# Optimization experiments

Hardware: AMD Instinct MI355X
Metric: run time of the kernel (lower is better)

Reference implementation:

```python
import jax, jax.numpy as jnp
import numpy as np

WINDOW = 7
SHIFT = 3
HEADS = 4


def _rel_pos_index(w):
    # same construction as ShiftedWindowAttention.__init__ (numpy, static)
    coords = np.stack(np.meshgrid(np.arange(w), np.arange(w), indexing='ij'))  # [2,w,w]
    cf = coords.reshape(2, -1)                       # [2, w*w]
    rc = (cf[:, :, None] - cf[:, None, :]).transpose(1, 2, 0)  # [L,L,2]
    rc[:, :, 0] += w - 1
    rc[:, :, 1] += w - 1
    rc[:, :, 0] *= 2 * w - 1
    return rc.sum(-1).reshape(-1)                    # [L*L]


def _attn_mask(H, W, w, s):
    # cyclic-shift attention mask, static numpy constant
    m = np.zeros((H, W))
    slices = ((0, -w), (-w, -s), (-s, None))
    cnt = 0
    for hs in slices:
        for ws in slices:
            m[hs[0]:hs[1], ws[0]:ws[1]] = cnt
            cnt += 1
    m = m.reshape(H // w, w, W // w, w).transpose(0, 2, 1, 3).reshape(-1, w * w)  # [nwin, L]
    d = m[:, None, :] - m[:, :, None]                # [nwin, L, L]
    return np.where(d != 0, -100.0, 0.0).astype(np.float32)


def setup_inputs() -> dict:
    key = jax.random.key(0)
    ks = jax.random.split(key, 6)
    B, H, W, C = 64, 56, 56, 128
    return {
        'x': jax.random.normal(ks[0], (B, H, W, C), dtype=jnp.float32),
        'qkv_weight': jax.random.normal(ks[1], (3 * C, C), dtype=jnp.float32) * 0.02,
        'qkv_bias': jax.random.normal(ks[2], (3 * C,), dtype=jnp.float32) * 0.02,
        'proj_weight': jax.random.normal(ks[3], (C, C), dtype=jnp.float32) * 0.02,
        'proj_bias': jax.random.normal(ks[4], (C,), dtype=jnp.float32) * 0.02,
        'rel_bias_table': jax.random.normal(ks[5], ((2 * WINDOW - 1) ** 2, HEADS), dtype=jnp.float32) * 0.02,
    }


def reference(x, qkv_weight, qkv_bias, proj_weight, proj_bias, rel_bias_table):
    B, H, W, C = x.shape
    w, s, h = WINDOW, SHIFT, HEADS
    d = C // h
    nH, nW = H // w, W // w
    nwin = nH * nW
    L = w * w

    # relative position bias: [h, L, L]
    bias = rel_bias_table[jnp.asarray(_rel_pos_index(w))].reshape(L, L, h).transpose(2, 0, 1)

    # cyclic shift + window partition -> [B*nwin, L, C]
    xs = jnp.roll(x, (-s, -s), axis=(1, 2))
    xw = xs.reshape(B, nH, w, nW, w, C).transpose(0, 1, 3, 2, 4, 5).reshape(B * nwin, L, C)

    # fused qkv projection (F.linear: x @ W.T + b)
    qkv = (xw @ qkv_weight.T + qkv_bias).reshape(B * nwin, L, 3, h, d).transpose(2, 0, 3, 1, 4)
    q, k, v = qkv[0] * (d ** -0.5), qkv[1], qkv[2]   # each [B*nwin, h, L, d]

    attn = jnp.einsum('nhqd,nhkd->nhqk', q, k) + bias[None]
    mask = jnp.asarray(_attn_mask(H, W, w, s))       # [nwin, L, L]
    attn = attn.reshape(B, nwin, h, L, L) + mask[None, :, None]
    attn = jax.nn.softmax(attn.reshape(B * nwin, h, L, L), axis=-1)

    out = jnp.einsum('nhqk,nhkd->nhqd', attn, v).transpose(0, 2, 1, 3).reshape(B * nwin, L, C)
    out = out @ proj_weight.T + proj_bias

    # window merge + reverse shift -> [B, H, W, C]
    out = out.reshape(B, nH, nW, w, w, C).transpose(0, 1, 3, 2, 4, 5).reshape(B, H, W, C)
    return jnp.roll(out, (s, s), axis=(1, 2))
```

## Files before the change

### kernel.cpp

```cpp
#include <hip/hip_runtime.h>

typedef __attribute__((ext_vector_type(8))) short short8;
typedef __attribute__((ext_vector_type(4))) float f32x4;

static __device__ __forceinline__ unsigned short f2bf(float f) {
  union { float f; unsigned int u; } v; v.f = f;
  unsigned int r = v.u + 0x7FFFu + ((v.u >> 16) & 1u);
  return (unsigned short)(r >> 16);
}
static __device__ __forceinline__ unsigned int pack2(float a, float b) {
  return (unsigned int)f2bf(a) | ((unsigned int)f2bf(b) << 16);
}

#define B1 0
#define B2 2560
#define WS2 5120

__global__ __launch_bounds__(256) void k_prep(const float* __restrict__ wq,
    const float* __restrict__ wp, const float* __restrict__ tbl,
    unsigned short* __restrict__ dq, unsigned short* __restrict__ dp,
    unsigned short* __restrict__ biasH) {
  const int n = blockIdx.x * 256 + threadIdx.x;
  if (n < 384 * 128) dq[n] = f2bf(wq[n]);
  if (n < 128 * 128) dp[n] = f2bf(wp[n]);
  if (n < 65536) {
    const int j = n & 63, i = (n >> 6) & 63;
    const int h = (n >> 12) & 3, bb = (n >> 14) & 1, aa = (n >> 15) & 1;
    float val;
    if (i >= 49) val = 0.0f;
    else if (j >= 49) val = -1e30f;
    else {
      const int ih = i / 7, iw = i - ih * 7, jh = j / 7, jw = j - jh * 7;
      const int didx = (ih - jh + 6) * 13 + (iw - jw + 6);
      const int irg = (aa ? (ih < 4 ? 3 : 6) : 0) + (bb ? (iw < 4 ? 1 : 2) : 0);
      const int jrg = (aa ? (jh < 4 ? 3 : 6) : 0) + (bb ? (jw < 4 ? 1 : 2) : 0);
      val = tbl[didx * 4 + h] - (irg != jrg ? 100.0f : 0.0f);
    }
    biasH[n] = f2bf(val);
  }
}

__global__ __launch_bounds__(256, 2) void k_fused(const float* __restrict__ x,
    const unsigned short* __restrict__ Wq, const float* __restrict__ qb,
    const unsigned short* __restrict__ Wp, const float* __restrict__ pb,
    const unsigned short* __restrict__ biasH, float* __restrict__ out) {
  __shared__ __align__(16) unsigned short lds[4 * WS2];
  const int tid = threadIdx.x;
  const int win = blockIdx.x;
  const int b = win >> 6, wl = win & 63;
  const int wh = wl >> 3, ww = wl & 7;
  const int wv = tid >> 6, ln = tid & 63;
  const int l15 = ln & 15, l4 = ln >> 4;
  unsigned short* W = lds + wv * WS2;

  const unsigned short* bmB = biasH
      + ((((wh == 7 ? 2 : 0) + (ww == 7 ? 1 : 0)) * 4 + wv) << 12)
      + l15 * 64 + 4 * l4;
  uint2 bm16[4][4];
#pragma unroll
  for (int mt = 0; mt < 4; ++mt)
#pragma unroll
    for (int nt = 0; nt < 4; ++nt)
      bm16[mt][nt] = *(const uint2*)(bmB + mt * 1024 + nt * 16);
  __builtin_amdgcn_sched_barrier(0);

  const float* rp[4];
  bool vld[4];
#pragma unroll
  for (int mt = 0; mt < 4; ++mt) {
    const int t = mt * 16 + l15;
    vld[mt] = (t < 49);
    const int tc = vld[mt] ? t : 0;
    const int th = tc / 7, tw = tc - th * 7;
    int sh = wh * 7 + th + 3; if (sh >= 56) sh -= 56;
    int sw = ww * 7 + tw + 3; if (sw >= 56) sw -= 56;
    rp[mt] = x + (((size_t)(b * 56 + sh)) * 56 + sw) * 128;
  }
  int nrow[6];
#pragma unroll
  for (int j = 0; j < 6; ++j)
    nrow[j] = (j >> 1) * 128 + wv * 32 + (j & 1) * 16 + l15;

  const f32x4 z4 = {0.f, 0.f, 0.f, 0.f};
  f32x4 aS[4][4], aV[4][2];
#pragma unroll
  for (int mt = 0; mt < 4; ++mt) {
#pragma unroll
    for (int j = 0; j < 4; ++j) aS[mt][j] = z4;
#pragma unroll
    for (int j = 0; j < 2; ++j) aV[mt][j] = z4;
  }
#pragma unroll
  for (int ks = 0; ks < 4; ++ks) {
    short8 af[4], bf[6];
#pragma unroll
    for (int mt = 0; mt < 4; ++mt) {
      const float4* p = (const float4*)(rp[mt] + ks * 32 + l4 * 8);
      float4 fa = p[0], fb = p[1];
      uint4 u;
      u.x = pack2(fa.x, fa.y); u.y = pack2(fa.z, fa.w);
      u.z = pack2(fb.x, fb.y); u.w = pack2(fb.z, fb.w);
      u.x = vld[mt] ? u.x : 0u; u.y = vld[mt] ? u.y : 0u;
      u.z = vld[mt] ? u.z : 0u; u.w = vld[mt] ? u.w : 0u;
      af[mt] = *(short8*)&u;
    }
#pragma unroll
    for (int j = 0; j < 6; ++j)
      bf[j] = *(const short8*)&Wq[(size_t)nrow[j] * 128 + ks * 32 + l4 * 8];
#pragma unroll
    for (int mt = 0; mt < 4; ++mt) {
#pragma unroll
      for (int j = 0; j < 4; ++j)
        aS[mt][j] = __builtin_amdgcn_mfma_f32_16x16x32_bf16(bf[j], af[mt], aS[mt][j], 0, 0, 0);
#pragma unroll
      for (int j = 0; j < 2; ++j)
        aV[mt][j] = __builtin_amdgcn_mfma_f32_16x16x32_bf16(af[mt], bf[4 + j], aV[mt][j], 0, 0, 0);
    }
  }
  {
    const float SC = 0.17677669529663687f;
    const float4 bq0 = *(const float4*)(qb + wv * 32 + 4 * l4);
    const float4 bq1 = *(const float4*)(qb + wv * 32 + 16 + 4 * l4);
    const float4 bk0 = *(const float4*)(qb + 128 + wv * 32 + 4 * l4);
    const float4 bk1 = *(const float4*)(qb + 128 + wv * 32 + 16 + 4 * l4);
#pragma unroll
    for (int mt = 0; mt < 4; ++mt) {
      const int t = mt * 16 + l15;
      uint2 u;
      u.x = pack2((aS[mt][0][0] + bq0.x) * SC, (aS[mt][0][1] + bq0.y) * SC);
      u.y = pack2((aS[mt][0][2] + bq0.z) * SC, (aS[mt][0][3] + bq0.w) * SC);
      *(uint2*)&W[B1 + t * 40 + 4 * l4] = u;
      u.x = pack2((aS[mt][1][0] + bq1.x) * SC, (aS[mt][1][1] + bq1.y) * SC);
      u.y = pack2((aS[mt][1][2] + bq1.z) * SC, (aS[mt][1][3] + bq1.w) * SC);
      *(uint2*)&W[B1 + t * 40 + 16 + 4 * l4] = u;
      u.x = pack2(aS[mt][2][0] + bk0.x, aS[mt][2][1] + bk0.y);
      u.y = pack2(aS[mt][2][2] + bk0.z, aS[mt][2][3] + bk0.w);
      *(uint2*)&W[B2 + t * 40 + 4 * l4] = u;
      u.x = pack2(aS[mt][3][0] + bk1.x, aS[mt][3][1] + bk1.y);
      u.y = pack2(aS[mt][3][2] + bk1.z, aS[mt][3][3] + bk1.w);
      *(uint2*)&W[B2 + t * 40 + 16 + 4 * l4] = u;
    }
  }

  f32x4 s[4][4];
#pragma unroll
  for (int mt = 0; mt < 4; ++mt)
#pragma unroll
    for (int nt = 0; nt < 4; ++nt) s[mt][nt] = z4;
  {
    short8 qf[4], kf[4];
#pragma unroll
    for (int mt = 0; mt < 4; ++mt)
      qf[mt] = *(const short8*)&W[B1 + (mt * 16 + l15) * 40 + l4 * 8];
#pragma unroll
    for (int nt = 0; nt < 4; ++nt)
      kf[nt] = *(const short8*)&W[B2 + (nt * 16 + l15) * 40 + l4 * 8];
    __builtin_amdgcn_s_setprio(1);
#pragma unroll
    for (int mt = 0; mt < 4; ++mt)
#pragma unroll
      for (int nt = 0; nt < 4; ++nt)
        s[mt][nt] = __builtin_amdgcn_mfma_f32_16x16x32_bf16(kf[nt], qf[mt], s[mt][nt], 0, 0, 0);
    __builtin_amdgcn_s_setprio(0);
  }
  {
    const float bv0 = qb[256 + wv * 32 + l15];
    const float bv1 = qb[256 + wv * 32 + 16 + l15];
#pragma unroll
    for (int mt = 0; mt < 4; ++mt) {
      uint2 u;
      u.x = pack2(aV[mt][0][0] + bv0, aV[mt][0][1] + bv0);
      u.y = pack2(aV[mt][0][2] + bv0, aV[mt][0][3] + bv0);
      *(uint2*)&W[B2 + l15 * 72 + mt * 16 + 4 * l4] = u;
      u.x = pack2(aV[mt][1][0] + bv1, aV[mt][1][1] + bv1);
      u.y = pack2(aV[mt][1][2] + bv1, aV[mt][1][3] + bv1);
      *(uint2*)&W[B2 + (16 + l15) * 72 + mt * 16 + 4 * l4] = u;
    }
  }

  float pmax[4] = {-1e30f, -1e30f, -1e30f, -1e30f};
#pragma unroll
  for (int mt = 0; mt < 4; ++mt) {
#pragma unroll
    for (int nt = 0; nt < 4; ++nt) {
      const uint2 u = bm16[mt][nt];
      const float b0 = __uint_as_float(u.x << 16);
      const float b1 = __uint_as_float(u.x & 0xFFFF0000u);
      const float b2 = __uint_as_float(u.y << 16);
      const float b3 = __uint_as_float(u.y & 0xFFFF0000u);
      s[mt][nt][0] += b0; s[mt][nt][1] += b1;
      s[mt][nt][2] += b2; s[mt][nt][3] += b3;
      pmax[mt] = fmaxf(pmax[mt], fmaxf(fmaxf(s[mt][nt][0], s[mt][nt][1]),
                                       fmaxf(s[mt][nt][2], s[mt][nt][3])));
    }
  }
  float inv[4];
#pragma unroll
  for (int mt = 0; mt < 4; ++mt) {
    float m0 = pmax[mt];
    m0 = fmaxf(m0, __shfl_xor(m0, 16));
    m0 = fmaxf(m0, __shfl_xor(m0, 32));
    float sum = 0.0f;
#pragma unroll
    for (int nt = 0; nt < 4; ++nt)
#pragma unroll
      for (int r = 0; r < 4; ++r) {
        const float v = s[mt][nt][r];
        const float e = (v > -1e29f) ? __expf(v - m0) : 0.0f;
        s[mt][nt][r] = e;
        sum += e;
      }
    sum += __shfl_xor(sum, 16);
    sum += __shfl_xor(sum, 32);
    inv[mt] = 1.0f / sum;
  }

  f32x4 o[4][2];
#pragma unroll
  for (int mt = 0; mt < 4; ++mt)
#pragma unroll
    for (int dt = 0; dt < 2; ++dt) o[mt][dt] = z4;
#pragma unroll
  for (int mt = 0; mt < 4; ++mt) {
    const int i = mt * 16 + l15;
    if (i < 49) {
#pragma unroll
      for (int nt = 0; nt < 2; ++nt) {
        uint2 u;
        u.x = pack2(s[mt][nt][0] * inv[mt], s[mt][nt][1] * inv[mt]);
        u.y = pack2(s[mt][nt][2] * inv[mt], s[mt][nt][3] * inv[mt]);
        *(uint2*)&W[B1 + i * 40 + nt * 16 + 4 * l4] = u;
      }
    }
  }
  {
    short8 pa[4], vb[2];
#pragma unroll
    for (int mt = 0; mt < 4; ++mt)
      pa[mt] = *(const short8*)&W[B1 + (mt * 16 + l15) * 40 + l4 * 8];
#pragma unroll
    for (int dt = 0; dt < 2; ++dt)
      vb[dt] = *(const short8*)&W[B2 + (dt * 16 + l15) * 72 + l4 * 8];
    __builtin_amdgcn_s_setprio(1);
#pragma unroll
    for (int mt = 0; mt < 4; ++mt)
#pragma unroll
      for (int dt = 0; dt < 2; ++dt)
        o[mt][dt] = __builtin_amdgcn_mfma_f32_16x16x32_bf16(vb[dt], pa[mt], o[mt][dt], 0, 0, 0);
    __builtin_amdgcn_s_setprio(0);
  }
#pragma unroll
  for (int mt = 0; mt < 4; ++mt) {
    const int i = mt * 16 + l15;
    if (i < 49) {
#pragma unroll
      for (int nt = 2; nt < 4; ++nt) {
        uint2 u;
        u.x = pack2(s[mt][nt][0] * inv[mt], s[mt][nt][1] * inv[mt]);
        u.y = pack2(s[mt][nt][2] * inv[mt], s[mt][nt][3] * inv[mt]);
        *(uint2*)&W[B1 + i * 40 + (nt - 2) * 16 + 4 * l4] = u;
      }
    }
  }
  {
    short8 pa[4], vb[2];
#pragma unroll
    for (int mt = 0; mt < 4; ++mt)
      pa[mt] = *(const short8*)&W[B1 + (mt * 16 + l15) * 40 + l4 * 8];
#pragma unroll
    for (int dt = 0; dt < 2; ++dt)
      vb[dt] = *(const short8*)&W[B2 + (dt * 16 + l15) * 72 + 32 + l4 * 8];
    __builtin_amdgcn_s_setprio(1);
#pragma unroll
    for (int mt = 0; mt < 4; ++mt)
#pragma unroll
      for (int dt = 0; dt < 2; ++dt)
        o[mt][dt] = __builtin_amdgcn_mfma_f32_16x16x32_bf16(vb[dt], pa[mt], o[mt][dt], 0, 0, 0);
    __builtin_amdgcn_s_setprio(0);
  }
#pragma unroll
  for (int mt = 0; mt < 4; ++mt) {
    const int t = mt * 16 + l15;
#pragma unroll
    for (int dt = 0; dt < 2; ++dt) {
      uint2 u;
      u.x = pack2(o[mt][dt][0], o[mt][dt][1]);
      u.y = pack2(o[mt][dt][2], o[mt][dt][3]);
      *(uint2*)&W[B1 + t * 40 + dt * 16 + 4 * l4] = u;
    }
  }
  __syncthreads();

  const float4 pbv0 = *(const float4*)(pb + wv * 32 + 4 * l4);
  const float4 pbv1 = *(const float4*)(pb + wv * 32 + 16 + 4 * l4);
  f32x4 c2[4][2];
#pragma unroll
  for (int mt = 0; mt < 4; ++mt)
#pragma unroll
    for (int nt = 0; nt < 2; ++nt) c2[mt][nt] = z4;
#pragma unroll
  for (int ks = 0; ks < 4; ++ks) {
    short8 a2[4], bp[2];
#pragma unroll
    for (int mt = 0; mt < 4; ++mt)
      a2[mt] = *(const short8*)&lds[ks * WS2 + B1 + (mt * 16 + l15) * 40 + l4 * 8];
#pragma unroll
    for (int nt = 0; nt < 2; ++nt)
      bp[nt] = *(const short8*)&Wp[(size_t)(wv * 32 + nt * 16 + l15) * 128 + ks * 32 + l4 * 8];
    __builtin_amdgcn_s_setprio(1);
#pragma unroll
    for (int mt = 0; mt < 4; ++mt)
#pragma unroll
      for (int nt = 0; nt < 2; ++nt)
        c2[mt][nt] = __builtin_amdgcn_mfma_f32_16x16x32_bf16(bp[nt], a2[mt], c2[mt][nt], 0, 0, 0);
    __builtin_amdgcn_s_setprio(0);
  }
#pragma unroll
  for (int mt = 0; mt < 4; ++mt) {
    const int t = mt * 16 + l15;
    if (t < 49) {
      const int th = t / 7, tw = t - th * 7;
      int y = wh * 7 + th + 3; if (y >= 56) y -= 56;
      int xx = ww * 7 + tw + 3; if (xx >= 56) xx -= 56;
      float* dstp = out + (((size_t)(b * 56 + y)) * 56 + xx) * 128 + wv * 32 + 4 * l4;
      float4 v0, v1;
      v0.x = c2[mt][0][0] + pbv0.x; v0.y = c2[mt][0][1] + pbv0.y;
      v0.z = c2[mt][0][2] + pbv0.z; v0.w = c2[mt][0][3] + pbv0.w;
      *(float4*)(dstp) = v0;
      v1.x = c2[mt][1][0] + pbv1.x; v1.y = c2[mt][1][1] + pbv1.y;
      v1.z = c2[mt][1][2] + pbv1.z; v1.w = c2[mt][1][3] + pbv1.w;
      *(float4*)(dstp + 16) = v1;
    }
  }
}

extern "C" void kernel_launch(void* const* d_in, const int* in_sizes, int n_in,
                              void* d_out, int out_size, void* d_ws, size_t ws_size,
                              hipStream_t stream) {
  const float* x     = (const float*)d_in[0];
  const float* qkvw  = (const float*)d_in[1];
  const float* qkvb  = (const float*)d_in[2];
  const float* projw = (const float*)d_in[3];
  const float* projb = (const float*)d_in[4];
  const float* table = (const float*)d_in[5];
  float* out = (float*)d_out;
  char* ws = (char*)d_ws;
  unsigned short* Wq    = (unsigned short*)ws;
  unsigned short* Wp    = (unsigned short*)(ws + 98304);
  unsigned short* biasH = (unsigned short*)(ws + 131072);

  k_prep<<<dim3(256), dim3(256), 0, stream>>>(qkvw, projw, table, Wq, Wp, biasH);
  k_fused<<<dim3(4096), dim3(256), 0, stream>>>(x, Wq, qkvb, Wp, projb, biasH, out);
}
```

Baseline: 176.6 us.

## Split each window's tokens across two waves per head, using 512-thread blocks

Each block now runs 8 waves instead of 4. Each head is handled by two waves, and each wave owns half of the 64 padded token rows. K and V are written to shared per-head LDS regions and combined with a block barrier, while each wave keeps a private Q/P buffer. The aim is to halve per-wave register and accumulator pressure and to raise wave-level parallelism and occupancy, so more memory latency is hidden. In exchange, every wave redundantly loads the same Wq fragments, an extra __syncthreads is added, and LDS per block grows.

```diff
diff --git a/kernel.cpp b/kernel.cpp
--- a/kernel.cpp
+++ b/kernel.cpp
@@ -12,9 +12,12 @@
   return (unsigned int)f2bf(a) | ((unsigned int)f2bf(b) << 16);
 }
 
-#define B1 0
-#define B2 2560
-#define WS2 5120
+#define QB_STR 1280
+#define KB_OFF 10240
+#define KB_STR 2560
+#define VB_OFF 20480
+#define VB_STR 2304
+#define LDS_SH 29696
 
 __global__ __launch_bounds__(256) void k_prep(const float* __restrict__ wq,
     const float* __restrict__ wp, const float* __restrict__ tbl,
@@ -40,35 +43,38 @@
   }
 }
 
-__global__ __launch_bounds__(256, 2) void k_fused(const float* __restrict__ x,
+__global__ __launch_bounds__(512, 4) void k_fused(const float* __restrict__ x,
     const unsigned short* __restrict__ Wq, const float* __restrict__ qb,
     const unsigned short* __restrict__ Wp, const float* __restrict__ pb,
     const unsigned short* __restrict__ biasH, float* __restrict__ out) {
-  __shared__ __align__(16) unsigned short lds[4 * WS2];
+  __shared__ __align__(16) unsigned short lds[LDS_SH];
   const int tid = threadIdx.x;
   const int win = blockIdx.x;
   const int b = win >> 6, wl = win & 63;
   const int wh = wl >> 3, ww = wl & 7;
-  const int wv = tid >> 6, ln = tid & 63;
+  const int w8 = tid >> 6, ln = tid & 63;
+  const int h = w8 & 3, half = w8 >> 2;
   const int l15 = ln & 15, l4 = ln >> 4;
-  unsigned short* W = lds + wv * WS2;
+  unsigned short* Qb = lds + w8 * QB_STR;
+  unsigned short* Kb = lds + KB_OFF + h * KB_STR;
+  unsigned short* Vb = lds + VB_OFF + h * VB_STR;
 
   const unsigned short* bmB = biasH
-      + ((((wh == 7 ? 2 : 0) + (ww == 7 ? 1 : 0)) * 4 + wv) << 12)
-      + l15 * 64 + 4 * l4;
-  uint2 bm16[4][4];
-#pragma unroll
-  for (int mt = 0; mt < 4; ++mt)
+      + ((((wh == 7 ? 2 : 0) + (ww == 7 ? 1 : 0)) * 4 + h) << 12)
+      + half * 2048 + l15 * 64 + 4 * l4;
+  uint2 bm16[2][4];
+#pragma unroll
+  for (int mt = 0; mt < 2; ++mt)
 #pragma unroll
     for (int nt = 0; nt < 4; ++nt)
       bm16[mt][nt] = *(const uint2*)(bmB + mt * 1024 + nt * 16);
   __builtin_amdgcn_sched_barrier(0);
 
-  const float* rp[4];
-  bool vld[4];
-#pragma unroll
-  for (int mt = 0; mt < 4; ++mt) {
-    const int t = mt * 16 + l15;
+  const float* rp[2];
+  bool vld[2];
+#pragma unroll
+  for (int mt = 0; mt < 2; ++mt) {
+    const int t = half * 32 + mt * 16 + l15;
     vld[mt] = (t < 49);
     const int tc = vld[mt] ? t : 0;
     const int th = tc / 7, tw = tc - th * 7;
@@ -79,12 +85,12 @@
   int nrow[6];
 #pragma unroll
   for (int j = 0; j < 6; ++j)
-    nrow[j] = (j >> 1) * 128 + wv * 32 + (j & 1) * 16 + l15;
+    nrow[j] = (j >> 1) * 128 + h * 32 + (j & 1) * 16 + l15;
 
   const f32x4 z4 = {0.f, 0.f, 0.f, 0.f};
-  f32x4 aS[4][4], aV[4][2];
-#pragma unroll
-  for (int mt = 0; mt < 4; ++mt) {
+  f32x4 aS[2][4], aV[2][2];
+#pragma unroll
+  for (int mt = 0; mt < 2; ++mt) {
 #pragma unroll
     for (int j = 0; j < 4; ++j) aS[mt][j] = z4;
 #pragma unroll
@@ -92,9 +98,9 @@
   }
 #pragma unroll
   for (int ks = 0; ks < 4; ++ks) {
-    short8 af[4], bf[6];
-#pragma unroll
-    for (int mt = 0; mt < 4; ++mt) {
+    short8 af[2], bf[6];
+#pragma unroll
+    for (int mt = 0; mt < 2; ++mt) {
       const float4* p = (const float4*)(rp[mt] + ks * 32 + l4 * 8);
       float4 fa = p[0], fb = p[1];
       uint4 u;
@@ -108,7 +114,7 @@
     for (int j = 0; j < 6; ++j)
       bf[j] = *(const short8*)&Wq[(size_t)nrow[j] * 128 + ks * 32 + l4 * 8];
 #pragma unroll
-    for (int mt = 0; mt < 4; ++mt) {
+    for (int mt = 0; mt < 2; ++mt) {
 #pragma unroll
       for (int j = 0; j < 4; ++j)
         aS[mt][j] = __builtin_amdgcn_mfma_f32_16x16x32_bf16(bf[j], af[mt], aS[mt][j], 0, 0, 0);
@@ -119,84 +125,78 @@
   }
   {
     const float SC = 0.17677669529663687f;
-    const float4 bq0 = *(const float4*)(qb + wv * 32 + 4 * l4);
-    const float4 bq1 = *(const float4*)(qb + wv * 32 + 16 + 4 * l4);
-    const float4 bk0 = *(const float4*)(qb + 128 + wv * 32 + 4 * l4);
-    const float4 bk1 = *(const float4*)(qb + 128 + wv * 32 + 16 + 4 * l4);
-#pragma unroll
-    for (int mt = 0; mt < 4; ++mt) {
-      const int t = mt * 16 + l15;
+    const float4 bq0 = *(const float4*)(qb + h * 32 + 4 * l4);
+    const float4 bq1 = *(const float4*)(qb + h * 32 + 16 + 4 * l4);
+    const float4 bk0 = *(const float4*)(qb + 128 + h * 32 + 4 * l4);
+    const float4 bk1 = *(const float4*)(qb + 128 + h * 32 + 16 + 4 * l4);
+    const float bv0 = qb[256 + h * 32 + l15];
+    const float bv1 = qb[256 + h * 32 + 16 + l15];
+#pragma unroll
+    for (int mt = 0; mt < 2; ++mt) {
+      const int tl = mt * 16 + l15;
+      const int tg = half * 32 + tl;
       uint2 u;
       u.x = pack2((aS[mt][0][0] + bq0.x) * SC, (aS[mt][0][1] + bq0.y) * SC);
       u.y = pack2((aS[mt][0][2] + bq0.z) * SC, (aS[mt][0][3] + bq0.w) * SC);
-      *(uint2*)&W[B1 + t * 40 + 4 * l4] = u;
+      *(uint2*)&Qb[tl * 40 + 4 * l4] = u;
       u.x = pack2((aS[mt][1][0] + bq1.x) * SC, (aS[mt][1][1] + bq1.y) * SC);
       u.y = pack2((aS[mt][1][2] + bq1.z) * SC, (aS[mt][1][3] + bq1.w) * SC);
-      *(uint2*)&W[B1 + t * 40 + 16 + 4 * l4] = u;
+      *(uint2*)&Qb[tl * 40 + 16 + 4 * l4] = u;
       u.x = pack2(aS[mt][2][0] + bk0.x, aS[mt][2][1] + bk0.y);
       u.y = pack2(aS[mt][2][2] + bk0.z, aS[mt][2][3] + bk0.w);
-      *(uint2*)&W[B2 + t * 40 + 4 * l4] = u;
+      *(uint2*)&Kb[tg * 40 + 4 * l4] = u;
       u.x = pack2(aS[mt][3][0] + bk1.x, aS[mt][3][1] + bk1.y);
       u.y = pack2(aS[mt][3][2] + bk1.z, aS[mt][3][3] + bk1.w);
-      *(uint2*)&W[B2 + t * 40 + 16 + 4 * l4] = u;
-    }
-  }
-
-  f32x4 s[4][4];
-#pragma unroll
-  for (int mt = 0; mt < 4; ++mt)
+      *(uint2*)&Kb[tg * 40 + 16 + 4 * l4] = u;
+      u.x = pack2(aV[mt][0][0] + bv0, aV[mt][0][1] + bv0);
+      u.y = pack2(aV[mt][0][2] + bv0, aV[mt][0][3] + bv0);
+      *(uint2*)&Vb[l15 * 72 + half * 32 + mt * 16 + 4 * l4] = u;
+      u.x = pack2(aV[mt][1][0] + bv1, aV[mt][1][1] + bv1);
+      u.y = pack2(aV[mt][1][2] + bv1, aV[mt][1][3] + bv1);
+      *(uint2*)&Vb[(16 + l15) * 72 + half * 32 + mt * 16 + 4 * l4] = u;
+    }
+  }
+  __syncthreads();
+
+  f32x4 s[2][4];
+#pragma unroll
+  for (int mt = 0; mt < 2; ++mt)
 #pragma unroll
     for (int nt = 0; nt < 4; ++nt) s[mt][nt] = z4;
   {
-    short8 qf[4], kf[4];
-#pragma unroll
-    for (int mt = 0; mt < 4; ++mt)
-      qf[mt] = *(const short8*)&W[B1 + (mt * 16 + l15) * 40 + l4 * 8];
+    short8 qf[2], kf[4];
+#pragma unroll
+    for (int mt = 0; mt < 2; ++mt)
+      qf[mt] = *(const short8*)&Qb[(mt * 16 + l15) * 40 + l4 * 8];
 #pragma unroll
     for (int nt = 0; nt < 4; ++nt)
-      kf[nt] = *(const short8*)&W[B2 + (nt * 16 + l15) * 40 + l4 * 8];
+      kf[nt] = *(const short8*)&Kb[(nt * 16 + l15) * 40 + l4 * 8];
     __builtin_amdgcn_s_setprio(1);
 #pragma unroll
-    for (int mt = 0; mt < 4; ++mt)
+    for (int mt = 0; mt < 2; ++mt)
 #pragma unroll
       for (int nt = 0; nt < 4; ++nt)
         s[mt][nt] = __builtin_amdgcn_mfma_f32_16x16x32_bf16(kf[nt], qf[mt], s[mt][nt], 0, 0, 0);
     __builtin_amdgcn_s_setprio(0);
   }
-  {
-    const float bv0 = qb[256 + wv * 32 + l15];
-    const float bv1 = qb[256 + wv * 32 + 16 + l15];
-#pragma unroll
-    for (int mt = 0; mt < 4; ++mt) {
-      uint2 u;
-      u.x = pack2(aV[mt][0][0] + bv0, aV[mt][0][1] + bv0);
-      u.y = pack2(aV[mt][0][2] + bv0, aV[mt][0][3] + bv0);
-      *(uint2*)&W[B2 + l15 * 72 + mt * 16 + 4 * l4] = u;
-      u.x = pack2(aV[mt][1][0] + bv1, aV[mt][1][1] + bv1);
-      u.y = pack2(aV[mt][1][2] + bv1, aV[mt][1][3] + bv1);
-      *(uint2*)&W[B2 + (16 + l15) * 72 + mt * 16 + 4 * l4] = u;
-    }
-  }
-
-  float pmax[4] = {-1e30f, -1e30f, -1e30f, -1e30f};
-#pragma unroll
-  for (int mt = 0; mt < 4; ++mt) {
+
+  float pmax[2] = {-1e30f, -1e30f};
+#pragma unroll
+  for (int mt = 0; mt < 2; ++mt) {
 #pragma unroll
     for (int nt = 0; nt < 4; ++nt) {
       const uint2 u = bm16[mt][nt];
-      const float b0 = __uint_as_float(u.x << 16);
-      const float b1 = __uint_as_float(u.x & 0xFFFF0000u);
-      const float b2 = __uint_as_float(u.y << 16);
-      const float b3 = __uint_as_float(u.y & 0xFFFF0000u);
-      s[mt][nt][0] += b0; s[mt][nt][1] += b1;
-      s[mt][nt][2] += b2; s[mt][nt][3] += b3;
+      s[mt][nt][0] += __uint_as_float(u.x << 16);
+      s[mt][nt][1] += __uint_as_float(u.x & 0xFFFF0000u);
+      s[mt][nt][2] += __uint_as_float(u.y << 16);
+      s[mt][nt][3] += __uint_as_float(u.y & 0xFFFF0000u);
       pmax[mt] = fmaxf(pmax[mt], fmaxf(fmaxf(s[mt][nt][0], s[mt][nt][1]),
                                        fmaxf(s[mt][nt][2], s[mt][nt][3])));
     }
   }
-  float inv[4];
-#pragma unroll
-  for (int mt = 0; mt < 4; ++mt) {
+  float inv[2];
+#pragma unroll
+  for (int mt = 0; mt < 2; ++mt) {
     float m0 = pmax[mt];
     m0 = fmaxf(m0, __shfl_xor(m0, 16));
     m0 = fmaxf(m0, __shfl_xor(m0, 32));
@@ -215,114 +215,87 @@
     inv[mt] = 1.0f / sum;
   }
 
-  f32x4 o[4][2];
-#pragma unroll
-  for (int mt = 0; mt < 4; ++mt)
+  f32x4 o[2][2];
+#pragma unroll
+  for (int mt = 0; mt < 2; ++mt)
 #pragma unroll
     for (int dt = 0; dt < 2; ++dt) o[mt][dt] = z4;
 #pragma unroll
-  for (int mt = 0; mt < 4; ++mt) {
-    const int i = mt * 16 + l15;
-    if (i < 49) {
-#pragma unroll
-      for (int nt = 0; nt < 2; ++nt) {
-        uint2 u;
-        u.x = pack2(s[mt][nt][0] * inv[mt], s[mt][nt][1] * inv[mt]);
-        u.y = pack2(s[mt][nt][2] * inv[mt], s[mt][nt][3] * inv[mt]);
-        *(uint2*)&W[B1 + i * 40 + nt * 16 + 4 * l4] = u;
+  for (int pass = 0; pass < 2; ++pass) {
+#pragma unroll
+    for (int mt = 0; mt < 2; ++mt) {
+      const int ig = half * 32 + mt * 16 + l15;
+      if (ig < 49) {
+#pragma unroll
+        for (int nt = 0; nt < 2; ++nt) {
+          const int ntp = pass * 2 + nt;
+          uint2 u;
+          u.x = pack2(s[mt][ntp][0] * inv[mt], s[mt][ntp][1] * inv[mt]);
+          u.y = pack2(s[mt][ntp][2] * inv[mt], s[mt][ntp][3] * inv[mt]);
+          *(uint2*)&Qb[(mt * 16 + l15) * 40 + nt * 16 + 4 * l4] = u;
+        }
       }
     }
-  }
-  {
-    short8 pa[4], vb[2];
-#pragma unroll
-    for (int mt = 0; mt < 4; ++mt)
-      pa[mt] = *(const short8*)&W[B1 + (mt * 16 + l15) * 40 + l4 * 8];
+    short8 pa[2], vb[2];
+#pragma unroll
+    for (int mt = 0; mt < 2; ++mt)
+      pa[mt] = *(const short8*)&Qb[(mt * 16 + l15) * 40 + l4 * 8];
 #pragma unroll
     for (int dt = 0; dt < 2; ++dt)
-      vb[dt] = *(const short8*)&W[B2 + (dt * 16 + l15) * 72 + l4 * 8];
+      vb[dt] = *(const short8*)&Vb[(dt * 16 + l15) * 72 + pass * 32 + l4 * 8];
     __builtin_amdgcn_s_setprio(1);
 #pragma unroll
-    for (int mt = 0; mt < 4; ++mt)
+    for (int mt = 0; mt < 2; ++mt)
 #pragma unroll
       for (int dt = 0; dt < 2; ++dt)
         o[mt][dt] = __builtin_amdgcn_mfma_f32_16x16x32_bf16(vb[dt], pa[mt], o[mt][dt], 0, 0, 0);
     __builtin_amdgcn_s_setprio(0);
   }
 #pragma unroll
-  for (int mt = 0; mt < 4; ++mt) {
-    const int i = mt * 16 + l15;
-    if (i < 49) {
-#pragma unroll
-      for (int nt = 2; nt < 4; ++nt) {
-        uint2 u;
-        u.x = pack2(s[mt][nt][0] * inv[mt], s[mt][nt][1] * inv[mt]);
-        u.y = pack2(s[mt][nt][2] * inv[mt], s[mt][nt][3] * inv[mt]);
-        *(uint2*)&W[B1 + i * 40 + (nt - 2) * 16 + 4 * l4] = u;
-      }
-    }
-  }
-  {
-    short8 pa[4], vb[2];
-#pragma unroll
-    for (int mt = 0; mt < 4; ++mt)
-      pa[mt] = *(const short8*)&W[B1 + (mt * 16 + l15) * 40 + l4 * 8];
-#pragma unroll
-    for (int dt = 0; dt < 2; ++dt)
-      vb[dt] = *(const short8*)&W[B2 + (dt * 16 + l15) * 72 + 32 + l4 * 8];
-    __builtin_amdgcn_s_setprio(1);
-#pragma unroll
-    for (int mt = 0; mt < 4; ++mt)
-#pragma unroll
-      for (int dt = 0; dt < 2; ++dt)
-        o[mt][dt] = __builtin_amdgcn_mfma_f32_16x16x32_bf16(vb[dt], pa[mt], o[mt][dt], 0, 0, 0);
-    __builtin_amdgcn_s_setprio(0);
-  }
-#pragma unroll
-  for (int mt = 0; mt < 4; ++mt) {
-    const int t = mt * 16 + l15;
+  for (int mt = 0; mt < 2; ++mt) {
+    const int tl = mt * 16 + l15;
 #pragma unroll
     for (int dt = 0; dt < 2; ++dt) {
       uint2 u;
       u.x = pack2(o[mt][dt][0], o[mt][dt][1]);
       u.y = pack2(o[mt][dt][2], o[mt][dt][3]);
-      *(uint2*)&W[B1 + t * 40 + dt * 16 + 4 * l4] = u;
+      *(uint2*)&Qb[tl * 40 + dt * 16 + 4 * l4] = u;
     }
   }
   __syncthreads();
 
-  const float4 pbv0 = *(const float4*)(pb + wv * 32 + 4 * l4);
-  const float4 pbv1 = *(const float4*)(pb + wv * 32 + 16 + 4 * l4);
-  f32x4 c2[4][2];
-#pragma unroll
-  for (int mt = 0; mt < 4; ++mt)
+  const float4 pbv0 = *(const float4*)(pb + h * 32 + 4 * l4);
+  const float4 pbv1 = *(const float4*)(pb + h * 32 + 16 + 4 * l4);
+  f32x4 c2[2][2];
+#pragma unroll
+  for (int mt = 0; mt < 2; ++mt)
 #pragma unroll
     for (int nt = 0; nt < 2; ++nt) c2[mt][nt] = z4;
 #pragma unroll
   for (int ks = 0; ks < 4; ++ks) {
-    short8 a2[4], bp[2];
-#pragma unroll
-    for (int mt = 0; mt < 4; ++mt)
-      a2[mt] = *(const short8*)&lds[ks * WS2 + B1 + (mt * 16 + l15) * 40 + l4 * 8];
+    short8 a2[2], bp[2];
+#pragma unroll
+    for (int mt = 0; mt < 2; ++mt)
+      a2[mt] = *(const short8*)&lds[(half * 4 + ks) * QB_STR + (mt * 16 + l15) * 40 + l4 * 8];
 #pragma unroll
     for (int nt = 0; nt < 2; ++nt)
-      bp[nt] = *(const short8*)&Wp[(size_t)(wv * 32 + nt * 16 + l15) * 128 + ks * 32 + l4 * 8];
+      bp[nt] = *(const short8*)&Wp[(size_t)(h * 32 + nt * 16 + l15) * 128 + ks * 32 + l4 * 8];
     __builtin_amdgcn_s_setprio(1);
 #pragma unroll
-    for (int mt = 0; mt < 4; ++mt)
+    for (int mt = 0; mt < 2; ++mt)
 #pragma unroll
       for (int nt = 0; nt < 2; ++nt)
         c2[mt][nt] = __builtin_amdgcn_mfma_f32_16x16x32_bf16(bp[nt], a2[mt], c2[mt][nt], 0, 0, 0);
     __builtin_amdgcn_s_setprio(0);
   }
 #pragma unroll
-  for (int mt = 0; mt < 4; ++mt) {
-    const int t = mt * 16 + l15;
+  for (int mt = 0; mt < 2; ++mt) {
+    const int t = half * 32 + mt * 16 + l15;
     if (t < 49) {
       const int th = t / 7, tw = t - th * 7;
       int y = wh * 7 + th + 3; if (y >= 56) y -= 56;
       int xx = ww * 7 + tw + 3; if (xx >= 56) xx -= 56;
-      float* dstp = out + (((size_t)(b * 56 + y)) * 56 + xx) * 128 + wv * 32 + 4 * l4;
+      float* dstp = out + (((size_t)(b * 56 + y)) * 56 + xx) * 128 + h * 32 + 4 * l4;
       float4 v0, v1;
       v0.x = c2[mt][0][0] + pbv0.x; v0.y = c2[mt][0][1] + pbv0.y;
       v0.z = c2[mt][0][2] + pbv0.z; v0.w = c2[mt][0][3] + pbv0.w;
@@ -350,5 +323,5 @@
   unsigned short* biasH = (unsigned short*)(ws + 131072);
 
   k_prep<<<dim3(256), dim3(256), 0, stream>>>(qkvw, projw, table, Wq, Wp, biasH);
-  k_fused<<<dim3(4096), dim3(256), 0, stream>>>(x, Wq, qkvb, Wp, projb, biasH, out);
-}
+  k_fused<<<dim3(4096), dim3(512), 0, stream>>>(x, Wq, qkvb, Wp, projb, biasH, out);
+}
```

After: 233.3 us. 1.32x slower.
